# Kernel optimization log

Measured on AMD Instinct MI355X. Metric: run time of the kernel, lower is better.

The kernel has to match this reference:

```python
import jax, jax.numpy as jnp
import numpy as np

B, T, C = 2, 2048, 2048
N_HEAD, N_KV = 16, 2
D_HEAD = C // N_HEAD          # 128
R = N_HEAD // N_KV            # q heads per kv head = 8


def setup_inputs() -> dict:
    key = jax.random.key(0)
    ks = jax.random.split(key, 5)
    s = 0.02
    return {
        "x": jax.random.normal(ks[0], (B, T, C), dtype=jnp.float32),
        "Wq": jax.random.normal(ks[1], (C, C), dtype=jnp.float32) * s,
        "Wk": jax.random.normal(ks[2], (C, N_KV * D_HEAD), dtype=jnp.float32) * s,
        "Wv": jax.random.normal(ks[3], (C, N_KV * D_HEAD), dtype=jnp.float32) * s,
        "Wo": jax.random.normal(ks[4], (C, C), dtype=jnp.float32) * s,
    }


def reference(x, Wq, Wk, Wv, Wo):
    b, t, c = x.shape
    # projections (no bias per config.bias=False)
    q = (x @ Wq).reshape(b, t, N_KV, R, D_HEAD)        # group q heads by kv group
    k = (x @ Wk).reshape(b, t, N_KV, D_HEAD)
    v = (x @ Wv).reshape(b, t, N_KV, D_HEAD)
    scale = 1.0 / jnp.sqrt(jnp.float32(D_HEAD))
    # scores: [b, g(kv), r, tq, tk] -- broadcast kv heads instead of repeat_interleave
    att = jnp.einsum('btgrd,bsgd->bgrts', q, k) * scale
    causal = jnp.tril(jnp.ones((t, t), dtype=bool))
    att = jnp.where(causal, att, -jnp.inf)
    att = jax.nn.softmax(att, axis=-1)
    y = jnp.einsum('bgrts,bsgd->btgrd', att, v).reshape(b, t, c)
    return y @ Wo
```

## Files before the change

### kernel.cpp

```cpp
#include <hip/hip_runtime.h>
#include <stdint.h>

using bf16x8 = __attribute__((ext_vector_type(8))) __bf16;
using f32x4  = __attribute__((ext_vector_type(4))) float;

#define GLL(g, l) __builtin_amdgcn_global_load_lds(                                  \
    (const __attribute__((address_space(1))) void*)(g),                              \
    (__attribute__((address_space(3))) void*)(l), 16, 0, 0)

__device__ __forceinline__ unsigned short f2bf(float f) {
  unsigned u = __builtin_bit_cast(unsigned, f);
  u += 0x7FFF + ((u >> 16) & 1);
  return (unsigned short)(u >> 16);
}
__device__ __forceinline__ float bf2f(unsigned short u) {
  unsigned v = ((unsigned)u) << 16;
  return __builtin_bit_cast(float, v);
}

__global__ __launch_bounds__(256) void cast_kernel(const float* __restrict__ in,
                                                   unsigned short* __restrict__ out, int n4) {
  int i = blockIdx.x * 256 + threadIdx.x;
  if (i >= n4) return;
  float4 v = reinterpret_cast<const float4*>(in)[i];
  ushort4 o;
  o.x = f2bf(v.x); o.y = f2bf(v.y); o.z = f2bf(v.z); o.w = f2bf(v.w);
  reinterpret_cast<ushort4*>(out)[i] = o;
}

__global__ __launch_bounds__(256) void tcast_kernel(const float* __restrict__ W,
                                                    unsigned short* __restrict__ Wt,
                                                    int K, int N) {
  __shared__ float T[64][65];
  const int k0 = blockIdx.x * 64, n0 = blockIdx.y * 64;
  const int t = threadIdx.x;
  const int r4 = t >> 6, c = t & 63;
#pragma unroll
  for (int p = 0; p < 16; ++p) {
    int r = p * 4 + r4;
    T[r][c] = W[(size_t)(k0 + r) * N + n0 + c];
  }
  __syncthreads();
#pragma unroll
  for (int p = 0; p < 16; ++p) {
    int r = p * 4 + r4;
    Wt[(size_t)(n0 + r) * K + k0 + c] = f2bf(T[c][r]);
  }
}

__global__ __launch_bounds__(256) void tv_kernel(const unsigned short* __restrict__ V,
                                                 unsigned short* __restrict__ Vt) {
  __shared__ unsigned short T[64][68];
  const int t0 = blockIdx.x * 64;
  const int d0 = blockIdx.y * 64;
  const int t = threadIdx.x;
  const int r4 = t >> 6, c = t & 63;
#pragma unroll
  for (int p = 0; p < 16; ++p) {
    int r = p * 4 + r4;
    T[r][c] = V[(size_t)(t0 + r) * 2560 + 2304 + d0 + c];
  }
  __syncthreads();
  const int b = t0 >> 11;
  const int tl = t0 & 2047;
#pragma unroll
  for (int p = 0; p < 16; ++p) {
    int dr = p * 4 + r4;
    int dg = d0 + dr;
    int g = dg >> 7, dl = dg & 127;
    Vt[(size_t)((b * 2 + g) * 128 + dl) * 2048 + tl + c] = T[c][dr];
  }
}

template <bool FP32OUT>
__global__ __launch_bounds__(256) void gemm_bt_kernel(const unsigned short* __restrict__ A,
                                                      const unsigned short* __restrict__ Bt,
                                                      void* __restrict__ Cout,
                                                      int K, int lda, int ldb, int ldc,
                                                      float scale, int nscale) {
  __shared__ __align__(16) unsigned short As[128 * 64];
  __shared__ __align__(16) unsigned short Bs[128 * 64];
  const int m0 = blockIdx.x * 128, n0 = blockIdx.y * 128;
  const int t = threadIdx.x;
  const int w = t >> 6, lane = t & 63;
  const int l15 = lane & 15, quad = lane >> 4;
  const int wm = (w >> 1) * 64, wn = (w & 1) * 64;

  const int srow = lane >> 3;
  const int sgl = (lane & 7) ^ srow;

  f32x4 acc[4][4] = {};

  for (int k0 = 0; k0 < K; k0 += 64) {
    __syncthreads();
#pragma unroll
    for (int p = 0; p < 4; ++p) {
      int rowbase = p * 32 + w * 8;
      GLL(&A[(size_t)(m0 + rowbase + srow) * lda + k0 + sgl * 8], &As[rowbase * 64]);
      GLL(&Bt[(size_t)(n0 + rowbase + srow) * ldb + k0 + sgl * 8], &Bs[rowbase * 64]);
    }
    __syncthreads();
#pragma unroll
    for (int kk = 0; kk < 64; kk += 32) {
      const int kg = kk >> 3;
      const int phys = ((kg + quad) ^ (l15 & 7)) * 8;
      bf16x8 af[4], bfr[4];
#pragma unroll
      for (int mt = 0; mt < 4; ++mt)
        af[mt] = *reinterpret_cast<const bf16x8*>(&As[(wm + mt * 16 + l15) * 64 + phys]);
#pragma unroll
      for (int nt = 0; nt < 4; ++nt)
        bfr[nt] = *reinterpret_cast<const bf16x8*>(&Bs[(wn + nt * 16 + l15) * 64 + phys]);
#pragma unroll
      for (int mt = 0; mt < 4; ++mt)
#pragma unroll
        for (int nt = 0; nt < 4; ++nt)
          acc[mt][nt] = __builtin_amdgcn_mfma_f32_16x16x32_bf16(af[mt], bfr[nt], acc[mt][nt], 0, 0, 0);
    }
  }

  const float sc = (n0 < nscale) ? scale : 1.0f;
#pragma unroll
  for (int mt = 0; mt < 4; ++mt) {
#pragma unroll
    for (int reg = 0; reg < 4; ++reg) {
      int row = m0 + wm + mt * 16 + quad * 4 + reg;
#pragma unroll
      for (int nt = 0; nt < 4; ++nt) {
        int col = n0 + wn + nt * 16 + l15;
        float v = acc[mt][nt][reg] * sc;
        if (FP32OUT)
          reinterpret_cast<float*>(Cout)[(size_t)row * ldc + col] = v;
        else
          reinterpret_cast<unsigned short*>(Cout)[(size_t)row * ldc + col] = f2bf(v);
      }
    }
  }
}

#define LDQK 2560
__global__ __launch_bounds__(256, 2) void attn_kernel(const unsigned short* __restrict__ Q,
                                                      const unsigned short* __restrict__ Kg,
                                                      const unsigned short* __restrict__ Vt,
                                                      float* __restrict__ O0,
                                                      unsigned short* __restrict__ O1,
                                                      float* __restrict__ L) {
  __shared__ __align__(16) unsigned short Ks[2][64 * 128];
  __shared__ __align__(16) unsigned short Vs[2][128 * 64];
  __shared__ __align__(16) unsigned short Pw[4][32 * 32];

  const int s  = blockIdx.x;
  const int bx = blockIdx.y;
  const int hh = blockIdx.z & 15;
  const int b  = blockIdx.z >> 4;
  const int g  = hh >> 3;
  const int t  = threadIdx.x;
  const int wg = t >> 6, lane = t & 63;
  const int l15 = lane & 15, quad = lane >> 4;

  const unsigned short* Kbase = Kg + (size_t)b * 2048 * LDQK + g * 128;
  const unsigned short* Vbase = Vt + (size_t)(b * 2 + g) * 128 * 2048;

  const int k_r = lane >> 4;
  const int v_r = lane >> 3;

  auto issueK = [&](int tile, unsigned short* dst) {
    const unsigned short* kb = Kbase + (size_t)(tile * 64) * LDQK;
#pragma unroll
    for (int p = 0; p < 4; ++p) {
      int rowbase = p * 16 + wg * 4;
      int row = rowbase + k_r;
      int gl = (lane & 15) ^ (row & 15);
      GLL(&kb[(size_t)row * LDQK + gl * 8], &dst[rowbase * 128]);
    }
  };
  auto issueV = [&](int tile, unsigned short* dst) {
    const unsigned short* vb = Vbase + tile * 64;
#pragma unroll
    for (int p = 0; p < 4; ++p) {
      int rowbase = p * 32 + wg * 8;
      int row = rowbase + v_r;
      int gl = (lane & 7) ^ (row & 7);
      GLL(&vb[(size_t)row * 2048 + gl * 8], &dst[rowbase * 64]);
    }
  };

  int pb = 0;
  issueK(s, Ks[0]);
  issueV(s, Vs[0]);

  for (int ph = 0; ph < 2; ++ph) {
    const int iq = ph ? (15 - bx) : bx;

    bf16x8 qf[2][4];
#pragma unroll
    for (int mi = 0; mi < 2; ++mi) {
      int qrow = iq * 128 + wg * 32 + mi * 16 + l15;
      const unsigned short* qp = &Q[(size_t)(b * 2048 + qrow) * LDQK + hh * 128 + quad * 8];
#pragma unroll
      for (int dk = 0; dk < 4; ++dk)
        qf[mi][dk] = *reinterpret_cast<const bf16x8*>(qp + dk * 32);
    }

    f32x4 o[2][8] = {};
    float l_run[2][4] = {};

    for (int j = 0; j <= iq; ++j) {
      const int tile = 2 * j + s;
      __syncthreads();
      const int cur = pb, nxt = pb ^ 1;

      if (j < iq) {
        issueK(tile + 2, Ks[nxt]);
        issueV(tile + 2, Vs[nxt]);
      } else if (ph == 0) {
        issueK(s, Ks[nxt]);
        issueV(s, Vs[nxt]);
      }

      f32x4 sc[2][4] = {};
#pragma unroll
      for (int nt = 0; nt < 4; ++nt) {
#pragma unroll
        for (int dk = 0; dk < 4; ++dk) {
          int phys = (dk * 4 + quad) ^ l15;
          bf16x8 kf = *reinterpret_cast<const bf16x8*>(&Ks[cur][(nt * 16 + l15) * 128 + phys * 8]);
          sc[0][nt] = __builtin_amdgcn_mfma_f32_16x16x32_bf16(qf[0][dk], kf, sc[0][nt], 0, 0, 0);
          sc[1][nt] = __builtin_amdgcn_mfma_f32_16x16x32_bf16(qf[1][dk], kf, sc[1][nt], 0, 0, 0);
        }
      }
      if (j == iq) {
#pragma unroll
        for (int mi = 0; mi < 2; ++mi)
#pragma unroll
          for (int nt = 0; nt < 4; ++nt) {
            int kcol = tile * 64 + nt * 16 + l15;
#pragma unroll
            for (int reg = 0; reg < 4; ++reg) {
              int qr = iq * 128 + wg * 32 + mi * 16 + quad * 4 + reg;
              if (kcol > qr) sc[mi][nt][reg] = -1e30f;
            }
          }
      }

#pragma unroll
      for (int kk = 0; kk < 2; ++kk) {
#pragma unroll
        for (int ntl = 0; ntl < 2; ++ntl) {
          const int nt = kk * 2 + ntl;
#pragma unroll
          for (int mi = 0; mi < 2; ++mi)
#pragma unroll
            for (int reg = 0; reg < 4; ++reg) {
              float p = __builtin_exp2f(__builtin_fmaf(sc[mi][nt][reg], 1.44269504f, -23.08312064f));
              l_run[mi][reg] += p;
              int row = mi * 16 + quad * 4 + reg;
              int slot = (ntl * 2 + (l15 >> 3)) ^ (row & 3);
              Pw[wg][row * 32 + slot * 8 + (l15 & 7)] = f2bf(p);
            }
        }
        bf16x8 pf[2];
#pragma unroll
        for (int mi = 0; mi < 2; ++mi) {
          int row = mi * 16 + l15;
          int slot = quad ^ (row & 3);
          pf[mi] = *reinterpret_cast<const bf16x8*>(&Pw[wg][row * 32 + slot * 8]);
        }
#pragma unroll
        for (int dt = 0; dt < 8; ++dt) {
          int phys = ((kk * 4 + quad) ^ (l15 & 7));
          bf16x8 vf = *reinterpret_cast<const bf16x8*>(&Vs[cur][(dt * 16 + l15) * 64 + phys * 8]);
#pragma unroll
          for (int mi = 0; mi < 2; ++mi)
            o[mi][dt] = __builtin_amdgcn_mfma_f32_16x16x32_bf16(pf[mi], vf, o[mi][dt], 0, 0, 0);
        }
      }
      pb ^= 1;
    }

#pragma unroll
    for (int off = 1; off <= 8; off <<= 1)
#pragma unroll
      for (int mi = 0; mi < 2; ++mi)
#pragma unroll
        for (int reg = 0; reg < 4; ++reg)
          l_run[mi][reg] += __shfl_xor(l_run[mi][reg], off);

#pragma unroll
    for (int mi = 0; mi < 2; ++mi)
#pragma unroll
      for (int reg = 0; reg < 4; ++reg) {
        int row = wg * 32 + mi * 16 + quad * 4 + reg;
        size_t base = (size_t)(b * 2048 + iq * 128 + row) * 2048 + hh * 128;
        if (s == 0) {
#pragma unroll
          for (int dt = 0; dt < 8; ++dt)
            O0[base + dt * 16 + l15] = o[mi][dt][reg];
        } else {
#pragma unroll
          for (int dt = 0; dt < 8; ++dt)
            O1[base + dt * 16 + l15] = f2bf(o[mi][dt][reg]);
        }
        if (l15 == 0)
          L[(size_t)s * 65536 + (size_t)(b * 2048 + iq * 128 + row) * 16 + hh] = l_run[mi][reg];
      }
  }
}

__global__ __launch_bounds__(256) void merge_kernel(const float* __restrict__ O0,
                                                    unsigned short* __restrict__ O1,
                                                    const float* __restrict__ L) {
  int i4 = blockIdx.x * 256 + threadIdx.x;
  int e = i4 << 2;
  int tr = e >> 11;
  int hh = (e >> 7) & 15;
  float l = L[tr * 16 + hh] + L[65536 + tr * 16 + hh];
  float inv = 1.0f / l;
  float4 a = reinterpret_cast<const float4*>(O0)[i4];
  ushort4 u = reinterpret_cast<const ushort4*>(O1)[i4];
  ushort4 r;
  r.x = f2bf((a.x + bf2f(u.x)) * inv);
  r.y = f2bf((a.y + bf2f(u.y)) * inv);
  r.z = f2bf((a.z + bf2f(u.z)) * inv);
  r.w = f2bf((a.w + bf2f(u.w)) * inv);
  reinterpret_cast<ushort4*>(O1)[i4] = r;
}

extern "C" void kernel_launch(void* const* d_in, const int* in_sizes, int n_in,
                              void* d_out, int out_size, void* d_ws, size_t ws_size,
                              hipStream_t stream) {
  const float* x  = (const float*)d_in[0];
  const float* Wq = (const float*)d_in[1];
  const float* Wk = (const float*)d_in[2];
  const float* Wv = (const float*)d_in[3];
  const float* Wo = (const float*)d_in[4];

  char* ws = (char*)d_ws;
  unsigned short* xb    = (unsigned short*)(ws + 0);
  unsigned short* Wqkvt = (unsigned short*)(ws + 16777216);
  unsigned short* Wot   = (unsigned short*)(ws + 27262976);
  unsigned short* QKVb  = (unsigned short*)(ws + 35651584);
  unsigned short* Vtb   = (unsigned short*)(ws + 56623104);
  float*          Lb    = (float*)(ws + 58720256);
  unsigned short* Yb    = xb;

  cast_kernel<<<8192, 256, 0, stream>>>(x, xb, 2097152);
  tcast_kernel<<<dim3(32, 32), 256, 0, stream>>>(Wq, Wqkvt, 2048, 2048);
  tcast_kernel<<<dim3(32, 4),  256, 0, stream>>>(Wk, Wqkvt + (size_t)2048 * 2048, 2048, 256);
  tcast_kernel<<<dim3(32, 4),  256, 0, stream>>>(Wv, Wqkvt + (size_t)2304 * 2048, 2048, 256);
  tcast_kernel<<<dim3(32, 32), 256, 0, stream>>>(Wo, Wot, 2048, 2048);

  const float qscale = 0.08838834764831845f;
  gemm_bt_kernel<false><<<dim3(32, 20), 256, 0, stream>>>(xb, Wqkvt, QKVb,
                                                          2048, 2048, 2048, 2560, qscale, 2048);
  tv_kernel<<<dim3(64, 4), 256, 0, stream>>>(QKVb, Vtb);
  attn_kernel<<<dim3(2, 8, 32), 256, 0, stream>>>(QKVb, QKVb + 2048, Vtb,
                                                  (float*)d_out, Yb, Lb);
  merge_kernel<<<8192, 256, 0, stream>>>((const float*)d_out, Yb, Lb);
  gemm_bt_kernel<true><<<dim3(32, 16), 256, 0, stream>>>(Yb, Wot, d_out,
                                                         2048, 2048, 2048, 2048, 1.0f, 0);
}
```

Before: 286.5 us.

## Compute S transposed and build P fragments in registers via permlane swaps

Swaps the MFMA operand order so the score tile comes out transposed: each lane holds a query row and four consecutive key columns. The exponentiated probabilities are packed to bf16 with v_cvt_pk_bf16_f32 and rearranged across lanes with v_permlane32/16_swap to form the PV A-operand directly. This removes the per-wave LDS round trip (scalar stores plus vector reads) for P. The row-sum reduction now needs only two cross-quad shuffles. The change relies on the exact permlane lane mapping matching the MFMA input layout; if that mapping is wrong the results are silently incorrect.

Result: no change. 282.3 us (-1.5%).

```diff
diff --git a/kernel.cpp b/kernel.cpp
--- a/kernel.cpp
+++ b/kernel.cpp
@@ -3,6 +3,7 @@
 
 using bf16x8 = __attribute__((ext_vector_type(8))) __bf16;
 using f32x4  = __attribute__((ext_vector_type(4))) float;
+using u32x4  = __attribute__((ext_vector_type(4))) unsigned;
 
 #define GLL(g, l) __builtin_amdgcn_global_load_lds(                                  \
     (const __attribute__((address_space(1))) void*)(g),                              \
@@ -147,7 +148,6 @@
                                                       float* __restrict__ L) {
   __shared__ __align__(16) unsigned short Ks[2][64 * 128];
   __shared__ __align__(16) unsigned short Vs[2][128 * 64];
-  __shared__ __align__(16) unsigned short Pw[4][32 * 32];
 
   const int s  = blockIdx.x;
   const int bx = blockIdx.y;
@@ -203,7 +203,7 @@
     }
 
     f32x4 o[2][8] = {};
-    float l_run[2][4] = {};
+    float l_run[2] = {};
 
     for (int j = 0; j <= iq; ++j) {
       const int tile = 2 * j + s;
@@ -225,8 +225,8 @@
         for (int dk = 0; dk < 4; ++dk) {
           int phys = (dk * 4 + quad) ^ l15;
           bf16x8 kf = *reinterpret_cast<const bf16x8*>(&Ks[cur][(nt * 16 + l15) * 128 + phys * 8]);
-          sc[0][nt] = __builtin_amdgcn_mfma_f32_16x16x32_bf16(qf[0][dk], kf, sc[0][nt], 0, 0, 0);
-          sc[1][nt] = __builtin_amdgcn_mfma_f32_16x16x32_bf16(qf[1][dk], kf, sc[1][nt], 0, 0, 0);
+          sc[0][nt] = __builtin_amdgcn_mfma_f32_16x16x32_bf16(kf, qf[0][dk], sc[0][nt], 0, 0, 0);
+          sc[1][nt] = __builtin_amdgcn_mfma_f32_16x16x32_bf16(kf, qf[1][dk], sc[1][nt], 0, 0, 0);
         }
       }
       if (j == iq) {
@@ -234,10 +234,10 @@
         for (int mi = 0; mi < 2; ++mi)
 #pragma unroll
           for (int nt = 0; nt < 4; ++nt) {
-            int kcol = tile * 64 + nt * 16 + l15;
 #pragma unroll
             for (int reg = 0; reg < 4; ++reg) {
-              int qr = iq * 128 + wg * 32 + mi * 16 + quad * 4 + reg;
+              int kcol = tile * 64 + nt * 16 + quad * 4 + reg;
+              int qr = iq * 128 + wg * 32 + mi * 16 + l15;
               if (kcol > qr) sc[mi][nt][reg] = -1e30f;
             }
           }
@@ -245,26 +245,31 @@
 
 #pragma unroll
       for (int kk = 0; kk < 2; ++kk) {
-#pragma unroll
-        for (int ntl = 0; ntl < 2; ++ntl) {
-          const int nt = kk * 2 + ntl;
-#pragma unroll
-          for (int mi = 0; mi < 2; ++mi)
-#pragma unroll
-            for (int reg = 0; reg < 4; ++reg) {
-              float p = __builtin_exp2f(__builtin_fmaf(sc[mi][nt][reg], 1.44269504f, -23.08312064f));
-              l_run[mi][reg] += p;
-              int row = mi * 16 + quad * 4 + reg;
-              int slot = (ntl * 2 + (l15 >> 3)) ^ (row & 3);
-              Pw[wg][row * 32 + slot * 8 + (l15 & 7)] = f2bf(p);
-            }
-        }
         bf16x8 pf[2];
 #pragma unroll
         for (int mi = 0; mi < 2; ++mi) {
-          int row = mi * 16 + l15;
-          int slot = quad ^ (row & 3);
-          pf[mi] = *reinterpret_cast<const bf16x8*>(&Pw[wg][row * 32 + slot * 8]);
+          float pe[4], po[4];
+#pragma unroll
+          for (int reg = 0; reg < 4; ++reg) {
+            pe[reg] = __builtin_exp2f(__builtin_fmaf(sc[mi][kk * 2 + 0][reg], 1.44269504f, -23.08312064f));
+            po[reg] = __builtin_exp2f(__builtin_fmaf(sc[mi][kk * 2 + 1][reg], 1.44269504f, -23.08312064f));
+            l_run[mi] += pe[reg] + po[reg];
+          }
+          unsigned a0, a1, b0, b1;
+          asm("v_cvt_pk_bf16_f32 %0, %1, %2" : "=v"(a0) : "v"(pe[0]), "v"(pe[1]));
+          asm("v_cvt_pk_bf16_f32 %0, %1, %2" : "=v"(a1) : "v"(pe[2]), "v"(pe[3]));
+          asm("v_cvt_pk_bf16_f32 %0, %1, %2" : "=v"(b0) : "v"(po[0]), "v"(po[1]));
+          asm("v_cvt_pk_bf16_f32 %0, %1, %2" : "=v"(b1) : "v"(po[2]), "v"(po[3]));
+          asm("v_permlane32_swap_b32 %0, %1" : "+v"(a0), "+v"(b0));
+          asm("v_permlane16_swap_b32 %0, %1" : "+v"(a0), "+v"(b0));
+          asm("v_permlane32_swap_b32 %0, %1" : "+v"(a1), "+v"(b1));
+          asm("v_permlane16_swap_b32 %0, %1" : "+v"(a1), "+v"(b1));
+          u32x4 w;
+          w[0] = a0;
+          w[1] = a1;
+          w[2] = b0;
+          w[3] = b1;
+          pf[mi] = __builtin_bit_cast(bf16x8, w);
         }
 #pragma unroll
         for (int dt = 0; dt < 8; ++dt) {
@@ -279,15 +284,17 @@
     }
 
 #pragma unroll
-    for (int off = 1; off <= 8; off <<= 1)
-#pragma unroll
-      for (int mi = 0; mi < 2; ++mi)
-#pragma unroll
-        for (int reg = 0; reg < 4; ++reg)
-          l_run[mi][reg] += __shfl_xor(l_run[mi][reg], off);
-
-#pragma unroll
-    for (int mi = 0; mi < 2; ++mi)
+    for (int mi = 0; mi < 2; ++mi) {
+      l_run[mi] += __shfl_xor(l_run[mi], 16);
+      l_run[mi] += __shfl_xor(l_run[mi], 32);
+    }
+
+#pragma unroll
+    for (int mi = 0; mi < 2; ++mi) {
+      if (quad == 0) {
+        int lrow = wg * 32 + mi * 16 + l15;
+        L[(size_t)s * 65536 + (size_t)(b * 2048 + iq * 128 + lrow) * 16 + hh] = l_run[mi];
+      }
 #pragma unroll
       for (int reg = 0; reg < 4; ++reg) {
         int row = wg * 32 + mi * 16 + quad * 4 + reg;
@@ -301,9 +308,8 @@
           for (int dt = 0; dt < 8; ++dt)
             O1[base + dt * 16 + l15] = f2bf(o[mi][dt][reg]);
         }
-        if (l15 == 0)
-          L[(size_t)s * 65536 + (size_t)(b * 2048 + iq * 128 + row) * 16 + hh] = l_run[mi][reg];
-      }
+      }
+    }
   }
 }
 
```
